# Optimization experiments

Measured on AMD Instinct MI355X. Metric: run time of the kernel, lower is better.

The kernel has to match this reference:

```python
import jax, jax.numpy as jnp
import numpy as np

NUM_NODES = 2048      # nodes per graph
N = 65536             # total nodes = 16 pairs * 2 graphs * 2048
E = 524288            # total edges
D = 128               # node_state_dim
ED = 64               # edge_encoded_dim
H = 256               # message_hidden_dim
M = 128               # message_dim
U = 256               # update_hidden_dim


def _mlp3(x, W1, b1, W2, b2, W3, b3):
    h = jax.nn.relu(x @ W1 + b1)
    h = jax.nn.relu(h @ W2 + b2)
    return h @ W3 + b3


def setup_inputs() -> dict:
    key = jax.random.key(0)
    ks = jax.random.split(key, 16)
    s = 0.02
    inp = {
        "node_states": jax.random.normal(ks[0], (N, D), jnp.float32),
        "edges": jax.random.normal(ks[1], (E, ED), jnp.float32),
        "vertices": jax.random.randint(ks[2], (E, 2), 0, N, jnp.int32),
        # message_encoder params
        "mW1": jax.random.normal(ks[3], (2 * D + ED, H), jnp.float32) * s,
        "mb1": jnp.zeros((H,), jnp.float32),
        "mW2": jax.random.normal(ks[4], (H, H), jnp.float32) * s,
        "mb2": jnp.zeros((H,), jnp.float32),
        "mW3": jax.random.normal(ks[5], (H, M), jnp.float32) * s,
        "mb3": jnp.zeros((M,), jnp.float32),
        # node_update params
        "uW1": jax.random.normal(ks[6], (D + M + D, U), jnp.float32) * s,
        "ub1": jnp.zeros((U,), jnp.float32),
        "uW2": jax.random.normal(ks[7], (U, U), jnp.float32) * s,
        "ub2": jnp.zeros((U,), jnp.float32),
        "uW3": jax.random.normal(ks[8], (U, D), jnp.float32) * s,
        "ub3": jnp.zeros((D,), jnp.float32),
    }
    return inp


def reference(node_states, edges, vertices,
              mW1, mb1, mW2, mb2, mW3, mb3,
              uW1, ub1, uW2, ub2, uW3, ub3):
    # gather endpoint states: [E, D] each
    nodes_i = node_states[vertices[:, 0]]
    nodes_j = node_states[vertices[:, 1]]
    # message MLP on [E, 2D+ED]
    messages = _mlp3(jnp.concatenate([nodes_i, nodes_j, edges], axis=1),
                     mW1, mb1, mW2, mb2, mW3, mb3)
    # scatter-add each message to BOTH endpoints (torch code repeats messages
    # twice and scatters by [v0; v1; arange] with zero padding for all nodes)
    summed = (jax.ops.segment_sum(messages, vertices[:, 0], num_segments=N)
              + jax.ops.segment_sum(messages, vertices[:, 1], num_segments=N))
    # cross-graph attention vectors: pairs of graphs, difference both ways
    paired = node_states.reshape(-1, 2, NUM_NODES, D)
    attention = jnp.concatenate([paired[:, 0] - paired[:, 1],
                                 paired[:, 1] - paired[:, 0]], axis=1).reshape(-1, D)
    upd_in = jnp.concatenate([node_states, summed, attention], axis=1)
    return _mlp3(upd_in, uW1, ub1, uW2, ub2, uW3, ub3)
```

## Files before the change

kernel.cpp:

```cpp
#include <hip/hip_runtime.h>

#define NNODES 65536
#define NEDGES 524288

typedef short bf16x8 __attribute__((ext_vector_type(8)));
typedef float f32x4 __attribute__((ext_vector_type(4)));

#define OF_MW1 0
#define OF_MW2 81920
#define OF_MW3 147456
#define OF_UW1 180224
#define OF_UW2 278528
#define OF_UW3 344064
#define WF_BYTES (376832 * 2)

#define WS_MSGS_BYTES ((size_t)NEDGES * 128 * 2)
#define WS_EIDX_OFF   WS_MSGS_BYTES
#define WS_EIDX_BYTES ((size_t)NNODES * 64 * 4)
#define WS_CNT_OFF    (WS_EIDX_OFF + WS_EIDX_BYTES)
#define WS_CNT_BYTES  ((size_t)NNODES * 4)
#define WS_WF_OFF     (WS_CNT_OFF + WS_CNT_BYTES)
#define WS_NEED       (WS_WF_OFF + WF_BYTES)

#define WS_SUMMED_BYTES ((size_t)NNODES * 128 * 4)

__device__ __forceinline__ unsigned short f2bf(float x) {
  unsigned int u = __float_as_uint(x);
  return (unsigned short)((u + 0x7FFFu + ((u >> 16) & 1u)) >> 16);
}

__device__ __forceinline__ float bf2f(short s) {
  return __uint_as_float((unsigned int)(unsigned short)s << 16);
}

__device__ __forceinline__ unsigned int cvtpk(float a, float b) {
  unsigned int r;
  asm("v_cvt_pk_bf16_f32 %0, %1, %2" : "=v"(r) : "v"(a), "v"(b));
  return r;
}

__device__ __forceinline__ void cvt_store8(unsigned short* p, float4 a, float4 b) {
  *reinterpret_cast<uint4*>(p) =
      make_uint4(cvtpk(a.x, a.y), cvtpk(a.z, a.w), cvtpk(b.x, b.y), cvtpk(b.z, b.w));
}

template <int MT, int KT, int NTW>
__device__ __forceinline__ void gemm_tile(const unsigned short* A, const int lda,
                                          const unsigned short* Wf,
                                          f32x4 (&acc)[MT][NTW], const int lane) {
  const int ar = lane & 15;
  const int ak = (lane >> 4) << 3;
  bf16x8 bcur[NTW], acur[MT];
#pragma unroll
  for (int n = 0; n < NTW; ++n)
    bcur[n] = *reinterpret_cast<const bf16x8*>(&Wf[(size_t)(n * KT) * 512 + lane * 8]);
#pragma unroll
  for (int m = 0; m < MT; ++m)
    acur[m] = *reinterpret_cast<const bf16x8*>(&A[(m * 16 + ar) * lda + ak]);
#pragma unroll
  for (int kt = 0; kt < KT; ++kt) {
    bf16x8 bnxt[NTW], anxt[MT];
    if (kt + 1 < KT) {
#pragma unroll
      for (int n = 0; n < NTW; ++n)
        bnxt[n] = *reinterpret_cast<const bf16x8*>(
            &Wf[(size_t)(n * KT + kt + 1) * 512 + lane * 8]);
#pragma unroll
      for (int m = 0; m < MT; ++m)
        anxt[m] = *reinterpret_cast<const bf16x8*>(
            &A[(m * 16 + ar) * lda + (kt + 1) * 32 + ak]);
    }
#pragma unroll
    for (int n = 0; n < NTW; ++n)
#pragma unroll
      for (int m = 0; m < MT; ++m)
        acc[m][n] = __builtin_amdgcn_mfma_f32_16x16x32_bf16(bcur[n], acur[m], acc[m][n], 0, 0, 0);
    if (kt + 1 < KT) {
#pragma unroll
      for (int n = 0; n < NTW; ++n) bcur[n] = bnxt[n];
#pragma unroll
      for (int m = 0; m < MT; ++m) acur[m] = anxt[m];
    }
  }
}

__global__ void prep_weights(const float* __restrict__ mW1, const float* __restrict__ mW2,
                             const float* __restrict__ mW3, const float* __restrict__ uW1,
                             const float* __restrict__ uW2, const float* __restrict__ uW3,
                             unsigned short* __restrict__ wf) {
  const int f = blockIdx.x;
  const int lane = threadIdx.x;
  const float* W; int NC, KT, fl, base;
  if (f < 160)      { W = mW1; NC = 256; KT = 10; fl = f;       base = OF_MW1; }
  else if (f < 288) { W = mW2; NC = 256; KT = 8;  fl = f - 160; base = OF_MW2; }
  else if (f < 352) { W = mW3; NC = 128; KT = 8;  fl = f - 288; base = OF_MW3; }
  else if (f < 544) { W = uW1; NC = 256; KT = 12; fl = f - 352; base = OF_UW1; }
  else if (f < 672) { W = uW2; NC = 256; KT = 8;  fl = f - 544; base = OF_UW2; }
  else              { W = uW3; NC = 128; KT = 8;  fl = f - 672; base = OF_UW3; }
  const int n_t = fl / KT;
  const int k_t = fl % KT;
  const int col = n_t * 16 + (lane & 15);
  const int krow = k_t * 32 + ((lane >> 4) << 3);
  unsigned short* dst = wf + base + (size_t)fl * 512 + lane * 8;
#pragma unroll
  for (int e = 0; e < 8; ++e) dst[e] = f2bf(W[(size_t)(krow + e) * NC + col]);
}

__global__ void fill_csr(const int* __restrict__ verts, int* __restrict__ cnt,
                         int* __restrict__ eidx) {
  const int k = blockIdx.x * 256 + threadIdx.x;
  const int v = verts[k];
  const int slot = atomicAdd(&cnt[v], 1);
  if (slot < 64) eidx[(size_t)v * 64 + slot] = k >> 1;
}

template <bool ATOMIC>
__global__ __launch_bounds__(256, 3) void msg_kernel(
    const float* __restrict__ ns, const float* __restrict__ edg,
    const int* __restrict__ verts, const unsigned short* __restrict__ wf,
    const float* __restrict__ mb1, const float* __restrict__ mb2,
    const float* __restrict__ mb3, float* __restrict__ summed,
    unsigned short* __restrict__ msgs) {
  extern __shared__ unsigned short smem[];
  unsigned short* Xs = smem;

  const int tid = threadIdx.x;
  const int lane = tid & 63;
  const int w = tid >> 6;
  const int e0 = blockIdx.x * 64;

  {
    const int r = tid >> 4;
    const int c = (tid & 15) * 8;
#pragma unroll
    for (int p = 0; p < 4; ++p) {
      const int row = p * 16 + r;
      const int2 vv = *reinterpret_cast<const int2*>(&verts[(size_t)(e0 + row) * 2]);
      const float4* s0 = reinterpret_cast<const float4*>(ns + (size_t)vv.x * 128 + c);
      cvt_store8(&Xs[row * 328 + c], s0[0], s0[1]);
      const float4* s1 = reinterpret_cast<const float4*>(ns + (size_t)vv.y * 128 + c);
      cvt_store8(&Xs[row * 328 + 128 + c], s1[0], s1[1]);
    }
#pragma unroll
    for (int i = tid; i < 512; i += 256) {
      const int row = i >> 3;
      const int cc = (i & 7) * 8;
      const float4* s2 = reinterpret_cast<const float4*>(edg + (size_t)(e0 + row) * 64 + cc);
      cvt_store8(&Xs[row * 328 + 256 + cc], s2[0], s2[1]);
    }
  }
  __syncthreads();

  const int cw = lane & 15;
  const int rq = (lane >> 4) * 4;

  {
    f32x4 acc[4][4];
#pragma unroll
    for (int m = 0; m < 4; ++m)
#pragma unroll
      for (int n = 0; n < 4; ++n)
#pragma unroll
        for (int i = 0; i < 4; ++i) acc[m][n][i] = 0.0f;
    gemm_tile<4, 10, 4>(Xs, 328, wf + OF_MW1 + (size_t)(w * 4) * 10 * 512, acc, lane);
    __syncthreads();
#pragma unroll
    for (int n = 0; n < 4; ++n) {
      const float4 bv = *reinterpret_cast<const float4*>(&mb1[w * 64 + n * 16 + rq]);
#pragma unroll
      for (int m = 0; m < 4; ++m) {
        const float x0 = fmaxf(acc[m][n][0] + bv.x, 0.0f);
        const float x1 = fmaxf(acc[m][n][1] + bv.y, 0.0f);
        const float x2 = fmaxf(acc[m][n][2] + bv.z, 0.0f);
        const float x3 = fmaxf(acc[m][n][3] + bv.w, 0.0f);
        *reinterpret_cast<uint2*>(&Xs[(m * 16 + cw) * 328 + w * 64 + n * 16 + rq]) =
            make_uint2(cvtpk(x0, x1), cvtpk(x2, x3));
      }
    }
  }
  __syncthreads();

  {
    f32x4 acc[4][4];
#pragma unroll
    for (int m = 0; m < 4; ++m)
#pragma unroll
      for (int n = 0; n < 4; ++n)
#pragma unroll
        for (int i = 0; i < 4; ++i) acc[m][n][i] = 0.0f;
    gemm_tile<4, 8, 4>(Xs, 328, wf + OF_MW2 + (size_t)(w * 4) * 8 * 512, acc, lane);
    __syncthreads();
#pragma unroll
    for (int n = 0; n < 4; ++n) {
      const float4 bv = *reinterpret_cast<const float4*>(&mb2[w * 64 + n * 16 + rq]);
#pragma unroll
      for (int m = 0; m < 4; ++m) {
        const float x0 = fmaxf(acc[m][n][0] + bv.x, 0.0f);
        const float x1 = fmaxf(acc[m][n][1] + bv.y, 0.0f);
        const float x2 = fmaxf(acc[m][n][2] + bv.z, 0.0f);
        const float x3 = fmaxf(acc[m][n][3] + bv.w, 0.0f);
        *reinterpret_cast<uint2*>(&Xs[(m * 16 + cw) * 328 + w * 64 + n * 16 + rq]) =
            make_uint2(cvtpk(x0, x1), cvtpk(x2, x3));
      }
    }
  }
  __syncthreads();

  {
    f32x4 acc[4][2];
#pragma unroll
    for (int m = 0; m < 4; ++m)
#pragma unroll
      for (int n = 0; n < 2; ++n)
#pragma unroll
        for (int i = 0; i < 4; ++i) acc[m][n][i] = 0.0f;
    gemm_tile<4, 8, 2>(Xs, 328, wf + OF_MW3 + (size_t)(w * 2) * 8 * 512, acc, lane);

    if constexpr (ATOMIC) {
#pragma unroll
      for (int n = 0; n < 2; ++n) {
        const float4 bv = *reinterpret_cast<const float4*>(&mb3[w * 32 + n * 16 + rq]);
        const float* bp = &bv.x;
#pragma unroll
        for (int m = 0; m < 4; ++m) {
          const int row = m * 16 + cw;
          const int2 vv = *reinterpret_cast<const int2*>(&verts[(size_t)(e0 + row) * 2]);
#pragma unroll
          for (int q = 0; q < 4; ++q) {
            const int col = w * 32 + n * 16 + rq + q;
            const float v = acc[m][n][q] + bp[q];
            unsafeAtomicAdd(&summed[(size_t)vv.x * 128 + col], v);
            unsafeAtomicAdd(&summed[(size_t)vv.y * 128 + col], v);
          }
        }
      }
    } else {
#pragma unroll
      for (int n = 0; n < 2; ++n) {
        const float4 bv = *reinterpret_cast<const float4*>(&mb3[w * 32 + n * 16 + rq]);
#pragma unroll
        for (int m = 0; m < 4; ++m) {
          *reinterpret_cast<uint2*>(
              &msgs[(size_t)(e0 + m * 16 + cw) * 128 + w * 32 + n * 16 + rq]) =
              make_uint2(cvtpk(acc[m][n][0] + bv.x, acc[m][n][1] + bv.y),
                         cvtpk(acc[m][n][2] + bv.z, acc[m][n][3] + bv.w));
        }
      }
    }
  }
}

template <bool GATHER>
__global__ __launch_bounds__(128, 3) void upd_kernel(
    const float* __restrict__ ns, const float* __restrict__ summed,
    const unsigned short* __restrict__ msgs, const int* __restrict__ cnt,
    const int* __restrict__ eidx, const unsigned short* __restrict__ wf,
    const float* __restrict__ ub1, const float* __restrict__ ub2,
    const float* __restrict__ ub3, float* __restrict__ out) {
  extern __shared__ unsigned short smem[];
  unsigned short* Xs = smem;

  const int tid = threadIdx.x;
  const int lane = tid & 63;
  const int w = tid >> 6;
  const int n0 = blockIdx.x * 32;

  for (int i = tid; i < 512; i += 128) {
    const int row = i >> 4;
    const int c = (i & 15) * 8;
    const int n = n0 + row;
    const float4* sA = reinterpret_cast<const float4*>(ns + (size_t)n * 128 + c);
    const float4 a0 = sA[0], a1 = sA[1];
    cvt_store8(&Xs[row * 392 + c], a0, a1);
    if constexpr (!GATHER) {
      const float4* sS = reinterpret_cast<const float4*>(summed + (size_t)n * 128 + c);
      cvt_store8(&Xs[row * 392 + 128 + c], sS[0], sS[1]);
    }
    const float4* sP = reinterpret_cast<const float4*>(ns + (size_t)(n ^ 2048) * 128 + c);
    const float4 p0 = sP[0], p1 = sP[1];
    float4 d0, d1;
    d0.x = a0.x - p0.x; d0.y = a0.y - p0.y; d0.z = a0.z - p0.z; d0.w = a0.w - p0.w;
    d1.x = a1.x - p1.x; d1.y = a1.y - p1.y; d1.z = a1.z - p1.z; d1.w = a1.w - p1.w;
    cvt_store8(&Xs[row * 392 + 256 + c], d0, d1);
  }

  if constexpr (GATHER) {
    for (int i = tid; i < 512; i += 128) {
      const int row = i >> 4;
      const int q4 = i & 15;
      reinterpret_cast<int4*>(&Xs[row * 392 + 128])[q4] =
          reinterpret_cast<const int4*>(&eidx[(size_t)(n0 + row) * 64])[q4];
    }
    __syncthreads();

    const int nl = tid >> 2;
    const int part = tid & 3;
    const int cn = min(cnt[n0 + nl], 64);
    const int* el = reinterpret_cast<const int*>(&Xs[nl * 392 + 128]);
    float acc[32];
#pragma unroll
    for (int k = 0; k < 32; ++k) acc[k] = 0.0f;
    for (int j = 0; j < cn; ++j) {
      const int e = el[j];
      const bf16x8* mp = reinterpret_cast<const bf16x8*>(&msgs[(size_t)e * 128 + part * 32]);
#pragma unroll
      for (int t = 0; t < 4; ++t) {
        const bf16x8 v = mp[t];
#pragma unroll
        for (int k = 0; k < 8; ++k) acc[t * 8 + k] += bf2f(v[k]);
      }
    }
    __syncthreads();
#pragma unroll
    for (int t = 0; t < 4; ++t) {
      *reinterpret_cast<uint4*>(&Xs[nl * 392 + 128 + part * 32 + t * 8]) =
          make_uint4(cvtpk(acc[t * 8 + 0], acc[t * 8 + 1]), cvtpk(acc[t * 8 + 2], acc[t * 8 + 3]),
                     cvtpk(acc[t * 8 + 4], acc[t * 8 + 5]), cvtpk(acc[t * 8 + 6], acc[t * 8 + 7]));
    }
  }
  __syncthreads();

  const int cw = lane & 15;
  const int rq = (lane >> 4) * 4;

  {
    f32x4 acc[2][8];
#pragma unroll
    for (int m = 0; m < 2; ++m)
#pragma unroll
      for (int n = 0; n < 8; ++n)
#pragma unroll
        for (int i = 0; i < 4; ++i) acc[m][n][i] = 0.0f;
    gemm_tile<2, 12, 8>(Xs, 392, wf + OF_UW1 + (size_t)(w * 8) * 12 * 512, acc, lane);
    __syncthreads();
#pragma unroll
    for (int n = 0; n < 8; ++n) {
      const float4 bv = *reinterpret_cast<const float4*>(&ub1[w * 128 + n * 16 + rq]);
#pragma unroll
      for (int m = 0; m < 2; ++m) {
        const float x0 = fmaxf(acc[m][n][0] + bv.x, 0.0f);
        const float x1 = fmaxf(acc[m][n][1] + bv.y, 0.0f);
        const float x2 = fmaxf(acc[m][n][2] + bv.z, 0.0f);
        const float x3 = fmaxf(acc[m][n][3] + bv.w, 0.0f);
        *reinterpret_cast<uint2*>(&Xs[(m * 16 + cw) * 392 + w * 128 + n * 16 + rq]) =
            make_uint2(cvtpk(x0, x1), cvtpk(x2, x3));
      }
    }
  }
  __syncthreads();

  {
    f32x4 acc[2][8];
#pragma unroll
    for (int m = 0; m < 2; ++m)
#pragma unroll
      for (int n = 0; n < 8; ++n)
#pragma unroll
        for (int i = 0; i < 4; ++i) acc[m][n][i] = 0.0f;
    gemm_tile<2, 8, 8>(Xs, 392, wf + OF_UW2 + (size_t)(w * 8) * 8 * 512, acc, lane);
    __syncthreads();
#pragma unroll
    for (int n = 0; n < 8; ++n) {
      const float4 bv = *reinterpret_cast<const float4*>(&ub2[w * 128 + n * 16 + rq]);
#pragma unroll
      for (int m = 0; m < 2; ++m) {
        const float x0 = fmaxf(acc[m][n][0] + bv.x, 0.0f);
        const float x1 = fmaxf(acc[m][n][1] + bv.y, 0.0f);
        const float x2 = fmaxf(acc[m][n][2] + bv.z, 0.0f);
        const float x3 = fmaxf(acc[m][n][3] + bv.w, 0.0f);
        *reinterpret_cast<uint2*>(&Xs[(m * 16 + cw) * 392 + w * 128 + n * 16 + rq]) =
            make_uint2(cvtpk(x0, x1), cvtpk(x2, x3));
      }
    }
  }
  __syncthreads();

  {
    f32x4 acc[2][4];
#pragma unroll
    for (int m = 0; m < 2; ++m)
#pragma unroll
      for (int n = 0; n < 4; ++n)
#pragma unroll
        for (int i = 0; i < 4; ++i) acc[m][n][i] = 0.0f;
    gemm_tile<2, 8, 4>(Xs, 392, wf + OF_UW3 + (size_t)(w * 4) * 8 * 512, acc, lane);
#pragma unroll
    for (int n = 0; n < 4; ++n) {
      const float4 bv = *reinterpret_cast<const float4*>(&ub3[w * 64 + n * 16 + rq]);
#pragma unroll
      for (int m = 0; m < 2; ++m) {
        const float4 o = make_float4(acc[m][n][0] + bv.x, acc[m][n][1] + bv.y,
                                     acc[m][n][2] + bv.z, acc[m][n][3] + bv.w);
        *reinterpret_cast<float4*>(
            &out[(size_t)(n0 + m * 16 + cw) * 128 + w * 64 + n * 16 + rq]) = o;
      }
    }
  }
}

extern "C" void kernel_launch(void* const* d_in, const int* in_sizes, int n_in,
                              void* d_out, int out_size, void* d_ws, size_t ws_size,
                              hipStream_t stream) {
  const float* ns   = (const float*)d_in[0];
  const float* edg  = (const float*)d_in[1];
  const int* verts  = (const int*)d_in[2];
  const float* mW1  = (const float*)d_in[3];
  const float* mb1  = (const float*)d_in[4];
  const float* mW2  = (const float*)d_in[5];
  const float* mb2  = (const float*)d_in[6];
  const float* mW3  = (const float*)d_in[7];
  const float* mb3  = (const float*)d_in[8];
  const float* uW1  = (const float*)d_in[9];
  const float* ub1  = (const float*)d_in[10];
  const float* uW2  = (const float*)d_in[11];
  const float* ub2  = (const float*)d_in[12];
  const float* uW3  = (const float*)d_in[13];
  const float* ub3  = (const float*)d_in[14];
  float* out = (float*)d_out;

  const int msg_lds = 64 * 328 * 2;
  const int upd_lds = 32 * 392 * 2;

  if (ws_size >= WS_NEED) {
    unsigned short* msgs = (unsigned short*)d_ws;
    int* eidx = (int*)((char*)d_ws + WS_EIDX_OFF);
    int* cnt  = (int*)((char*)d_ws + WS_CNT_OFF);
    unsigned short* wf = (unsigned short*)((char*)d_ws + WS_WF_OFF);

    (void)hipMemsetAsync(cnt, 0, WS_CNT_BYTES, stream);
    prep_weights<<<736, 64, 0, stream>>>(mW1, mW2, mW3, uW1, uW2, uW3, wf);
    fill_csr<<<2 * NEDGES / 256, 256, 0, stream>>>(verts, cnt, eidx);
    msg_kernel<false><<<NEDGES / 64, 256, msg_lds, stream>>>(
        ns, edg, verts, wf, mb1, mb2, mb3, nullptr, msgs);
    upd_kernel<true><<<NNODES / 32, 128, upd_lds, stream>>>(
        ns, nullptr, msgs, cnt, eidx, wf, ub1, ub2, ub3, out);
  } else {
    float* summed = (float*)d_ws;
    unsigned short* wf = (unsigned short*)((char*)d_ws + WS_SUMMED_BYTES);

    (void)hipMemsetAsync(summed, 0, WS_SUMMED_BYTES, stream);
    prep_weights<<<736, 64, 0, stream>>>(mW1, mW2, mW3, uW1, uW2, uW3, wf);
    msg_kernel<true><<<NEDGES / 64, 256, msg_lds, stream>>>(
        ns, edg, verts, wf, mb1, mb2, mb3, summed, nullptr);
    upd_kernel<false><<<NNODES / 32, 128, upd_lds, stream>>>(
        ns, summed, nullptr, nullptr, nullptr, wf, ub1, ub2, ub3, out);
  }
}
```

Before: 522.4 us.

## Swizzle message-kernel LDS layout, double-buffer weight loads, raise occupancy

Replaces the padded 328-element LDS row stride in the message kernel with an unpadded 320 stride plus an XOR swizzle on 16-byte chunks. This shrinks LDS per block while still avoiding bank conflicts. The GEMM tile now prefetches weight fragments two k-steps ahead using alternating B register buffers to hide global/L2 latency. Message kernel launch bounds go from 3 to 4 blocks per SM. The deeper prefetch and higher occupancy target may raise register pressure or cause spills.

```diff
diff --git a/kernel.cpp b/kernel.cpp
--- a/kernel.cpp
+++ b/kernel.cpp
@@ -2,6 +2,7 @@
 
 #define NNODES 65536
 #define NEDGES 524288
+#define MSG_LDA 320
 
 typedef short bf16x8 __attribute__((ext_vector_type(8)));
 typedef float f32x4 __attribute__((ext_vector_type(4)));
@@ -44,40 +45,65 @@
       make_uint4(cvtpk(a.x, a.y), cvtpk(a.z, a.w), cvtpk(b.x, b.y), cvtpk(b.z, b.w));
 }
 
-template <int MT, int KT, int NTW>
+__device__ __forceinline__ unsigned short* xswz(unsigned short* Xs, int row, int col) {
+  return reinterpret_cast<unsigned short*>(
+      reinterpret_cast<char*>(Xs) + (((row * MSG_LDA + col) * 2) ^ ((row & 7) << 4)));
+}
+__device__ __forceinline__ const unsigned short* xswz(const unsigned short* Xs, int row,
+                                                      int col) {
+  return reinterpret_cast<const unsigned short*>(
+      reinterpret_cast<const char*>(Xs) + (((row * MSG_LDA + col) * 2) ^ ((row & 7) << 4)));
+}
+
+template <int MT, int KT, int NTW, bool SWZ>
 __device__ __forceinline__ void gemm_tile(const unsigned short* A, const int lda,
                                           const unsigned short* Wf,
                                           f32x4 (&acc)[MT][NTW], const int lane) {
   const int ar = lane & 15;
   const int ak = (lane >> 4) << 3;
-  bf16x8 bcur[NTW], acur[MT];
-#pragma unroll
-  for (int n = 0; n < NTW; ++n)
-    bcur[n] = *reinterpret_cast<const bf16x8*>(&Wf[(size_t)(n * KT) * 512 + lane * 8]);
-#pragma unroll
-  for (int m = 0; m < MT; ++m)
-    acur[m] = *reinterpret_cast<const bf16x8*>(&A[(m * 16 + ar) * lda + ak]);
+
+  auto ldA = [&](int m, int kt) -> bf16x8 {
+    if constexpr (SWZ)
+      return *reinterpret_cast<const bf16x8*>(xswz(A, m * 16 + ar, kt * 32 + ak));
+    else
+      return *reinterpret_cast<const bf16x8*>(&A[(m * 16 + ar) * lda + kt * 32 + ak]);
+  };
+  auto ldB = [&](int n, int kt) -> bf16x8 {
+    return *reinterpret_cast<const bf16x8*>(&Wf[(size_t)(n * KT + kt) * 512 + lane * 8]);
+  };
+
+  bf16x8 b0[NTW], b1[NTW], acur[MT];
+#pragma unroll
+  for (int n = 0; n < NTW; ++n) b0[n] = ldB(n, 0);
+  if constexpr (KT > 1) {
+#pragma unroll
+    for (int n = 0; n < NTW; ++n) b1[n] = ldB(n, 1);
+  }
+#pragma unroll
+  for (int m = 0; m < MT; ++m) acur[m] = ldA(m, 0);
+
 #pragma unroll
   for (int kt = 0; kt < KT; ++kt) {
     bf16x8 bnxt[NTW], anxt[MT];
+    if (kt + 2 < KT) {
+#pragma unroll
+      for (int n = 0; n < NTW; ++n) bnxt[n] = ldB(n, kt + 2);
+    }
     if (kt + 1 < KT) {
 #pragma unroll
-      for (int n = 0; n < NTW; ++n)
-        bnxt[n] = *reinterpret_cast<const bf16x8*>(
-            &Wf[(size_t)(n * KT + kt + 1) * 512 + lane * 8]);
+      for (int m = 0; m < MT; ++m) anxt[m] = ldA(m, kt + 1);
+    }
+    bf16x8 (&bc)[NTW] = (kt & 1) ? b1 : b0;
+#pragma unroll
+    for (int n = 0; n < NTW; ++n)
 #pragma unroll
       for (int m = 0; m < MT; ++m)
-        anxt[m] = *reinterpret_cast<const bf16x8*>(
-            &A[(m * 16 + ar) * lda + (kt + 1) * 32 + ak]);
-    }
-#pragma unroll
-    for (int n = 0; n < NTW; ++n)
-#pragma unroll
-      for (int m = 0; m < MT; ++m)
-        acc[m][n] = __builtin_amdgcn_mfma_f32_16x16x32_bf16(bcur[n], acur[m], acc[m][n], 0, 0, 0);
+        acc[m][n] = __builtin_amdgcn_mfma_f32_16x16x32_bf16(bc[n], acur[m], acc[m][n], 0, 0, 0);
+    if (kt + 2 < KT) {
+#pragma unroll
+      for (int n = 0; n < NTW; ++n) bc[n] = bnxt[n];
+    }
     if (kt + 1 < KT) {
-#pragma unroll
-      for (int n = 0; n < NTW; ++n) bcur[n] = bnxt[n];
 #pragma unroll
       for (int m = 0; m < MT; ++m) acur[m] = anxt[m];
     }
@@ -115,7 +141,7 @@
 }
 
 template <bool ATOMIC>
-__global__ __launch_bounds__(256, 3) void msg_kernel(
+__global__ __launch_bounds__(256, 4) void msg_kernel(
     const float* __restrict__ ns, const float* __restrict__ edg,
     const int* __restrict__ verts, const unsigned short* __restrict__ wf,
     const float* __restrict__ mb1, const float* __restrict__ mb2,
@@ -137,16 +163,16 @@
       const int row = p * 16 + r;
       const int2 vv = *reinterpret_cast<const int2*>(&verts[(size_t)(e0 + row) * 2]);
       const float4* s0 = reinterpret_cast<const float4*>(ns + (size_t)vv.x * 128 + c);
-      cvt_store8(&Xs[row * 328 + c], s0[0], s0[1]);
+      cvt_store8(xswz(Xs, row, c), s0[0], s0[1]);
       const float4* s1 = reinterpret_cast<const float4*>(ns + (size_t)vv.y * 128 + c);
-      cvt_store8(&Xs[row * 328 + 128 + c], s1[0], s1[1]);
+      cvt_store8(xswz(Xs, row, 128 + c), s1[0], s1[1]);
     }
 #pragma unroll
     for (int i = tid; i < 512; i += 256) {
       const int row = i >> 3;
       const int cc = (i & 7) * 8;
       const float4* s2 = reinterpret_cast<const float4*>(edg + (size_t)(e0 + row) * 64 + cc);
-      cvt_store8(&Xs[row * 328 + 256 + cc], s2[0], s2[1]);
+      cvt_store8(xswz(Xs, row, 256 + cc), s2[0], s2[1]);
     }
   }
   __syncthreads();
@@ -162,7 +188,7 @@
       for (int n = 0; n < 4; ++n)
 #pragma unroll
         for (int i = 0; i < 4; ++i) acc[m][n][i] = 0.0f;
-    gemm_tile<4, 10, 4>(Xs, 328, wf + OF_MW1 + (size_t)(w * 4) * 10 * 512, acc, lane);
+    gemm_tile<4, 10, 4, true>(Xs, MSG_LDA, wf + OF_MW1 + (size_t)(w * 4) * 10 * 512, acc, lane);
     __syncthreads();
 #pragma unroll
     for (int n = 0; n < 4; ++n) {
@@ -173,7 +199,7 @@
         const float x1 = fmaxf(acc[m][n][1] + bv.y, 0.0f);
         const float x2 = fmaxf(acc[m][n][2] + bv.z, 0.0f);
         const float x3 = fmaxf(acc[m][n][3] + bv.w, 0.0f);
-        *reinterpret_cast<uint2*>(&Xs[(m * 16 + cw) * 328 + w * 64 + n * 16 + rq]) =
+        *reinterpret_cast<uint2*>(xswz(Xs, m * 16 + cw, w * 64 + n * 16 + rq)) =
             make_uint2(cvtpk(x0, x1), cvtpk(x2, x3));
       }
     }
@@ -188,7 +214,7 @@
       for (int n = 0; n < 4; ++n)
 #pragma unroll
         for (int i = 0; i < 4; ++i) acc[m][n][i] = 0.0f;
-    gemm_tile<4, 8, 4>(Xs, 328, wf + OF_MW2 + (size_t)(w * 4) * 8 * 512, acc, lane);
+    gemm_tile<4, 8, 4, true>(Xs, MSG_LDA, wf + OF_MW2 + (size_t)(w * 4) * 8 * 512, acc, lane);
     __syncthreads();
 #pragma unroll
     for (int n = 0; n < 4; ++n) {
@@ -199,7 +225,7 @@
         const float x1 = fmaxf(acc[m][n][1] + bv.y, 0.0f);
         const float x2 = fmaxf(acc[m][n][2] + bv.z, 0.0f);
         const float x3 = fmaxf(acc[m][n][3] + bv.w, 0.0f);
-        *reinterpret_cast<uint2*>(&Xs[(m * 16 + cw) * 328 + w * 64 + n * 16 + rq]) =
+        *reinterpret_cast<uint2*>(xswz(Xs, m * 16 + cw, w * 64 + n * 16 + rq)) =
             make_uint2(cvtpk(x0, x1), cvtpk(x2, x3));
       }
     }
@@ -214,7 +240,7 @@
       for (int n = 0; n < 2; ++n)
 #pragma unroll
         for (int i = 0; i < 4; ++i) acc[m][n][i] = 0.0f;
-    gemm_tile<4, 8, 2>(Xs, 328, wf + OF_MW3 + (size_t)(w * 2) * 8 * 512, acc, lane);
+    gemm_tile<4, 8, 2, true>(Xs, MSG_LDA, wf + OF_MW3 + (size_t)(w * 2) * 8 * 512, acc, lane);
 
     if constexpr (ATOMIC) {
 #pragma unroll
@@ -331,7 +357,7 @@
       for (int n = 0; n < 8; ++n)
 #pragma unroll
         for (int i = 0; i < 4; ++i) acc[m][n][i] = 0.0f;
-    gemm_tile<2, 12, 8>(Xs, 392, wf + OF_UW1 + (size_t)(w * 8) * 12 * 512, acc, lane);
+    gemm_tile<2, 12, 8, false>(Xs, 392, wf + OF_UW1 + (size_t)(w * 8) * 12 * 512, acc, lane);
     __syncthreads();
 #pragma unroll
     for (int n = 0; n < 8; ++n) {
@@ -357,7 +383,7 @@
       for (int n = 0; n < 8; ++n)
 #pragma unroll
         for (int i = 0; i < 4; ++i) acc[m][n][i] = 0.0f;
-    gemm_tile<2, 8, 8>(Xs, 392, wf + OF_UW2 + (size_t)(w * 8) * 8 * 512, acc, lane);
+    gemm_tile<2, 8, 8, false>(Xs, 392, wf + OF_UW2 + (size_t)(w * 8) * 8 * 512, acc, lane);
     __syncthreads();
 #pragma unroll
     for (int n = 0; n < 8; ++n) {
@@ -383,7 +409,7 @@
       for (int n = 0; n < 4; ++n)
 #pragma unroll
         for (int i = 0; i < 4; ++i) acc[m][n][i] = 0.0f;
-    gemm_tile<2, 8, 4>(Xs, 392, wf + OF_UW3 + (size_t)(w * 4) * 8 * 512, acc, lane);
+    gemm_tile<2, 8, 4, false>(Xs, 392, wf + OF_UW3 + (size_t)(w * 4) * 8 * 512, acc, lane);
 #pragma unroll
     for (int n = 0; n < 4; ++n) {
       const float4 bv = *reinterpret_cast<const float4*>(&ub3[w * 64 + n * 16 + rq]);
@@ -418,7 +444,7 @@
   const float* ub3  = (const float*)d_in[14];
   float* out = (float*)d_out;
 
-  const int msg_lds = 64 * 328 * 2;
+  const int msg_lds = 64 * MSG_LDA * 2;
   const int upd_lds = 32 * 392 * 2;
 
   if (ws_size >= WS_NEED) {
```

After: 675.3 us. +29.3%, slower.
